# Performance work log

Measured on AMD Instinct MI355X. Metric: run time of the kernel, lower is better.

Reference implementation:

```python
import jax, jax.numpy as jnp
import numpy as np

NUM_HEADS = 16
SIZE_PER_HEAD = 64
NEG_INF = -10000.0

def setup_inputs() -> dict:
    key = jax.random.key(0)
    ks = jax.random.split(key, 4)
    B, S, D = 4, 2048, 1024
    x = jax.random.normal(ks[0], (B, S, D), dtype=jnp.float32)
    mask = jnp.ones((B, S), dtype=jnp.int32)
    std = 0.02
    Wq = jax.random.normal(ks[1], (D, NUM_HEADS * SIZE_PER_HEAD), dtype=jnp.float32) * std
    Wk = jax.random.normal(ks[2], (D, NUM_HEADS * SIZE_PER_HEAD), dtype=jnp.float32) * std
    Wv = jax.random.normal(ks[3], (D, NUM_HEADS * SIZE_PER_HEAD), dtype=jnp.float32) * std
    bq = jnp.zeros((NUM_HEADS * SIZE_PER_HEAD,), dtype=jnp.float32)
    bk = jnp.zeros((NUM_HEADS * SIZE_PER_HEAD,), dtype=jnp.float32)
    bv = jnp.zeros((NUM_HEADS * SIZE_PER_HEAD,), dtype=jnp.float32)
    return {"x": x, "mask": mask, "Wq": Wq, "bq": bq, "Wk": Wk, "bk": bk, "Wv": Wv, "bv": bv}

def reference(x, mask, Wq, bq, Wk, bk, Wv, bv):
    B, S, D = x.shape
    H, Dh = NUM_HEADS, SIZE_PER_HEAD
    # QKV projections (no activations: query/key/value_activation default None)
    q = (x @ Wq + bq).reshape(B, S, H, Dh).transpose(0, 2, 1, 3)  # [B,H,S,Dh]
    k = (x @ Wk + bk).reshape(B, S, H, Dh).transpose(0, 2, 1, 3)
    v = (x @ Wv + bv).reshape(B, S, H, Dh).transpose(0, 2, 1, 3)
    scores = jnp.einsum('bhqd,bhkd->bhqk', q, k) / jnp.sqrt(jnp.float32(Dh))  # [B,H,S,S]
    # additive mask: (1 - mask) * neg_inf, broadcast over heads and query dim
    adder = (1.0 - mask.astype(jnp.float32))[:, None, None, :] * NEG_INF
    probs = jax.nn.softmax(scores + adder, axis=-1)
    # dropout is identity at inference (training=None)
    ctx = jnp.einsum('bhqk,bhkd->bhqd', probs, v)  # [B,H,S,Dh]
    return ctx.transpose(0, 2, 1, 3).reshape(B, S, H * Dh)
```

## Files before the change

kernel.cpp:

```cpp
#include <hip/hip_runtime.h>


typedef __attribute__((ext_vector_type(8))) short bf16x8;
typedef __attribute__((ext_vector_type(4))) float f32x4;
typedef __attribute__((ext_vector_type(16))) float f32x16;

#define LOG2E 1.4426950408889634f

__device__ __forceinline__ ushort f2bf(float f) {
  union { float f; unsigned int u; } x; x.f = f;
  unsigned int r = x.u + 0x7fffu + ((x.u >> 16) & 1u);
  return (ushort)(r >> 16);
}

__device__ __forceinline__ void gload16(const ushort* g, ushort* l) {
  __builtin_amdgcn_global_load_lds(
      (__attribute__((address_space(1))) unsigned int*)(g),
      (__attribute__((address_space(3))) unsigned int*)(l), 16, 0, 0);
}

__global__ __launch_bounds__(256) void prep(
    const float* __restrict__ x, ushort* __restrict__ xb,
    const float* __restrict__ Wq, const float* __restrict__ Wk,
    const float* __restrict__ Wv, ushort* __restrict__ WT,
    const int* __restrict__ mask, int* __restrict__ flagw) {
  __shared__ float tile[32][33];
  __shared__ int accum[64];
  const int blk = blockIdx.x, t = threadIdx.x;
  if (blk < 8192) {
    int i = blk * 256 + t;
    float4 v = ((const float4*)x)[i];
    ushort4 o;
    o.x = f2bf(v.x); o.y = f2bf(v.y); o.z = f2bf(v.z); o.w = f2bf(v.w);
    ((ushort4*)xb)[i] = o;
  } else if (blk < 11264) {
    int bb = blk - 8192;
    int z = bb >> 10, rem = bb & 1023, db = rem >> 5, nb = rem & 31;
    const float* W = (z == 0) ? Wq : ((z == 1) ? Wk : Wv);
    int tx = t & 31, ty = t >> 5;
#pragma unroll
    for (int i = 0; i < 4; i++) {
      int dl = ty + i * 8;
      tile[dl][tx] = W[(size_t)(db * 32 + dl) * 1024 + nb * 32 + tx];
    }
    __syncthreads();
#pragma unroll
    for (int i = 0; i < 4; i++) {
      int nl = ty + i * 8;
      WT[(size_t)(z * 1024 + nb * 32 + nl) * 1024 + db * 32 + tx] = f2bf(tile[tx][nl]);
    }
  } else {
    if (t < 64) accum[t] = 0;
    __syncthreads();
    int p = t >> 2, j = t & 3;
    int base = p * 128 + j * 32;
    int s = 0;
#pragma unroll
    for (int i = 0; i < 8; i++) {
      int4 v = *(const int4*)(mask + base + i * 4);
      s += v.x + v.y + v.z + v.w;
    }
    atomicAdd(&accum[p], s);
    __syncthreads();
    if (t < 4) {
      int w = 0;
#pragma unroll
      for (int kt = 0; kt < 16; kt++)
        if (accum[t * 16 + kt] != 128) w |= (1 << kt);
      flagw[t] = w;
    }
  }
}

__global__ __launch_bounds__(256, 2) void gemm_qkv(
    const ushort* __restrict__ xb, const ushort* __restrict__ WT,
    const float* __restrict__ bq, const float* __restrict__ bk,
    const float* __restrict__ bv, ushort* __restrict__ Qg,
    ushort* __restrict__ Kg, ushort* __restrict__ VTg) {
  __shared__ __align__(16) ushort As[128 * 64];
  __shared__ __align__(16) ushort Bs[128 * 64];
  const int t = threadIdx.x, wid = t >> 6, lane = t & 63;
  const int blk = blockIdx.x;
  int mode, mb, nb;
  const ushort *A, *B;
  if (blk < 1024) {
    mode = 0;
    int lin2 = (blk & 7) * 128 + (blk >> 3);
    nb = lin2 & 15; mb = lin2 >> 4;
    A = xb; B = WT;
  } else {
    mode = 1;
    int l = blk - 1024;
    int lin2 = (l & 7) * 64 + (l >> 3);
    mb = lin2 & 7; nb = lin2 >> 3;
    A = WT + (size_t)2048 * 1024; B = xb;
  }
  const ushort* Ab = A + (size_t)mb * 128 * 1024;
  const ushort* Bb = B + (size_t)nb * 128 * 1024;
  const int wr = wid >> 1, wc = wid & 1;

  f32x4 acc[4][4] = {};

  const int srow = lane >> 3;
  const int schunk = (lane & 7) ^ srow;

#pragma unroll
  for (int i = 0; i < 4; i++) {
    int blki = i * 4 + wid;
    int row = blki * 8 + srow;
    int ldso = __builtin_amdgcn_readfirstlane(blki * 512);
    gload16(Ab + (size_t)row * 1024 + schunk * 8, As + ldso);
    gload16(Bb + (size_t)row * 1024 + schunk * 8, Bs + ldso);
  }

  for (int kt = 0; kt < 16; ++kt) {
    __syncthreads();

    bf16x8 af[2][4], bf[2][4];
#pragma unroll
    for (int ks = 0; ks < 2; ks++) {
#pragma unroll
      for (int m = 0; m < 4; m++) {
        int row = wr * 64 + m * 16 + (lane & 15);
        int slot = (ks * 4 + (lane >> 4)) ^ (row & 7);
        af[ks][m] = *(const bf16x8*)(As + row * 64 + slot * 8);
      }
#pragma unroll
      for (int n = 0; n < 4; n++) {
        int row = wc * 64 + n * 16 + (lane & 15);
        int slot = (ks * 4 + (lane >> 4)) ^ (row & 7);
        bf[ks][n] = *(const bf16x8*)(Bs + row * 64 + slot * 8);
      }
    }
    __syncthreads();

    if (kt < 15) {
      const int kof = (kt + 1) * 64 + schunk * 8;
#pragma unroll
      for (int i = 0; i < 4; i++) {
        int blki = i * 4 + wid;
        int row = blki * 8 + srow;
        int ldso = __builtin_amdgcn_readfirstlane(blki * 512);
        gload16(Ab + (size_t)row * 1024 + kof, As + ldso);
        gload16(Bb + (size_t)row * 1024 + kof, Bs + ldso);
      }
    }

#pragma unroll
    for (int ks = 0; ks < 2; ks++)
#pragma unroll
      for (int m = 0; m < 4; m++)
#pragma unroll
        for (int n = 0; n < 4; n++)
          acc[m][n] = __builtin_amdgcn_mfma_f32_16x16x32_bf16(
              af[ks][m], bf[ks][n], acc[m][n], 0, 0, 0);
  }

#pragma unroll
  for (int m = 0; m < 4; m++) {
#pragma unroll
    for (int n = 0; n < 4; n++) {
      if (mode == 0) {
        int col = nb * 128 + wc * 64 + n * 16 + (lane & 15);
        int wq = col >> 10;
        float bs = wq ? bk[col & 1023] : bq[col & 1023];
        float scale = wq ? 1.0f : (0.125f * LOG2E);
        ushort* dst = wq ? Kg : Qg;
        int h = (col >> 6) & 15, d = col & 63;
#pragma unroll
        for (int r = 0; r < 4; r++) {
          int row = mb * 128 + wr * 64 + m * 16 + (lane >> 4) * 4 + r;
          int b = row >> 11, s = row & 2047;
          float v = (acc[m][n][r] + bs) * scale;
          dst[((size_t)((b << 4) + h) * 2048 + s) * 64 + d] = f2bf(v);
        }
      } else {
        int col = nb * 128 + wc * 64 + n * 16 + (lane & 15);
        int b = col >> 11, s = col & 2047;
#pragma unroll
        for (int r = 0; r < 4; r++) {
          int p = mb * 128 + wr * 64 + m * 16 + (lane >> 4) * 4 + r;
          float v = acc[m][n][r] + bv[p];
          int h = p >> 6, d = p & 63;
          VTg[((size_t)((b << 4) + h) * 64 + d) * 2048 + s] = f2bf(v);
        }
      }
    }
  }
}

__global__ __launch_bounds__(256, 3) void attn_kernel(
    const ushort* __restrict__ Qg, const ushort* __restrict__ Kg,
    const ushort* __restrict__ VTg, const int* __restrict__ mask,
    const int* __restrict__ flagw, float* __restrict__ out) {
  __shared__ __align__(16) ushort Ks[128 * 64];
  __shared__ __align__(16) ushort Vs[64 * 128];
  __shared__ float maddv[128];

  const int t = threadIdx.x, wid = t >> 6, lane = t & 63;
  const int l31 = lane & 31, hi = lane >> 5;
  const int lin = blockIdx.x;
  const int lin2 = (lin & 7) * 128 + (lin >> 3);
  const int qb = lin2 & 15, bh = lin2 >> 4;
  const int b = bh >> 4, h = bh & 15;
  const ushort* Qbh = Qg + ((size_t)bh * 2048 + qb * 128) * 64;
  const ushort* Kbh = Kg + (size_t)bh * 2048 * 64;
  const ushort* Vbh = VTg + (size_t)bh * 64 * 2048;

  const int pr_l = lane >> 4;
  const int s_l = lane & 15;

  const int prq = l31 >> 1;
  const int halfq = l31 & 1;
  const int pr14 = prq & 15;

#pragma unroll
  for (int i = 0; i < 4; i++) {
    int blki = i * 4 + wid;
    int ldso = __builtin_amdgcn_readfirstlane(blki * 512);
    int pr = blki * 4 + pr_l;
    int sp = s_l ^ (pr & 15);
    gload16(Qbh + (size_t)(2 * pr + (sp >> 3)) * 64 + (sp & 7) * 8, Ks + ldso);
  }
  const int fb = flagw[b];
  __syncthreads();
  bf16x8 qf[4];
  {
    const ushort* qbase = Ks + (wid * 16 + prq) * 128;
#pragma unroll
    for (int ds = 0; ds < 4; ds++) {
      int slot = ((ds * 2 + hi) | (halfq << 3)) ^ pr14;
      qf[ds] = *(const bf16x8*)(qbase + slot * 8);
    }
  }
  __syncthreads();

  const f32x16 fzero = {};
  f32x16 cacc[2] = {};
  float l0 = 0.f, l1 = 0.f, l2 = 0.f, l3 = 0.f;

  for (int kt = 0; kt < 16; ++kt) {
    {
#pragma unroll
      for (int i = 0; i < 4; i++) {
        int blki = i * 4 + wid;
        int ldso = __builtin_amdgcn_readfirstlane(blki * 512);
        int pr = blki * 4 + pr_l;
        int sp = s_l ^ (pr & 15);
        gload16(Kbh + (size_t)(kt * 128 + 2 * pr + (sp >> 3)) * 64 + (sp & 7) * 8,
                Ks + ldso);
      }
      int d_l = lane >> 4, c_s = lane & 15;
#pragma unroll
      for (int i = 0; i < 4; i++) {
        int blki = i * 4 + wid;
        int ldso = __builtin_amdgcn_readfirstlane(blki * 512);
        int d = blki * 4 + d_l;
        int cvg = c_s ^ (d & 15);
        gload16(Vbh + (size_t)d * 2048 + kt * 128 + cvg * 8, Vs + ldso);
      }
    }
    const bool msk = ((fb >> kt) & 1) != 0;
    if (msk && t < 128)
      maddv[t] = (1.0f - (float)mask[b * 2048 + kt * 128 + t]) * (-10000.0f * LOG2E);
    __syncthreads();

#pragma unroll
    for (int kb = 0; kb < 4; kb++) {
      const ushort* krow = Ks + (kb * 16 + prq) * 128;
      __builtin_amdgcn_s_setprio(1);
      bf16x8 kf0 = *(const bf16x8*)(krow + (((0 + hi) | (halfq << 3)) ^ pr14) * 8);
      f32x16 a = __builtin_amdgcn_mfma_f32_32x32x16_bf16(kf0, qf[0], fzero, 0, 0, 0);
      bf16x8 kf1 = *(const bf16x8*)(krow + (((2 + hi) | (halfq << 3)) ^ pr14) * 8);
      a = __builtin_amdgcn_mfma_f32_32x32x16_bf16(kf1, qf[1], a, 0, 0, 0);
      bf16x8 kf2 = *(const bf16x8*)(krow + (((4 + hi) | (halfq << 3)) ^ pr14) * 8);
      a = __builtin_amdgcn_mfma_f32_32x32x16_bf16(kf2, qf[2], a, 0, 0, 0);
      bf16x8 kf3 = *(const bf16x8*)(krow + (((6 + hi) | (halfq << 3)) ^ pr14) * 8);
      a = __builtin_amdgcn_mfma_f32_32x32x16_bf16(kf3, qf[3], a, 0, 0, 0);
      __builtin_amdgcn_s_setprio(0);

      if (msk) {
#pragma unroll
        for (int qd = 0; qd < 4; qd++) {
          f32x4 ma = *(const f32x4*)(maddv + kb * 32 + qd * 8 + hi * 4);
#pragma unroll
          for (int rr = 0; rr < 4; rr++) a[qd * 4 + rr] += ma[rr];
        }
      }

#pragma unroll
      for (int w2 = 0; w2 < 2; w2++) {
        const int o = w2 * 8;
        float e0 = __builtin_amdgcn_exp2f(a[o + 0]);
        float e1 = __builtin_amdgcn_exp2f(a[o + 1]);
        float e2 = __builtin_amdgcn_exp2f(a[o + 2]);
        float e3 = __builtin_amdgcn_exp2f(a[o + 3]);
        float e4 = __builtin_amdgcn_exp2f(a[o + 4]);
        float e5 = __builtin_amdgcn_exp2f(a[o + 5]);
        float e6 = __builtin_amdgcn_exp2f(a[o + 6]);
        float e7 = __builtin_amdgcn_exp2f(a[o + 7]);
        l0 += e0; l1 += e1; l2 += e2; l3 += e3;
        l0 += e4; l1 += e5; l2 += e6; l3 += e7;
        unsigned a0, a1, b0, b1;
        asm("v_cvt_pk_bf16_f32 %0, %1, %2" : "=v"(a0) : "v"(e0), "v"(e1));
        asm("v_cvt_pk_bf16_f32 %0, %1, %2" : "=v"(a1) : "v"(e2), "v"(e3));
        asm("v_cvt_pk_bf16_f32 %0, %1, %2" : "=v"(b0) : "v"(e4), "v"(e5));
        asm("v_cvt_pk_bf16_f32 %0, %1, %2" : "=v"(b1) : "v"(e6), "v"(e7));
        asm("v_permlane32_swap_b32 %0, %1" : "+v"(a0), "+v"(b0));
        asm("v_permlane32_swap_b32 %0, %1" : "+v"(a1), "+v"(b1));
        union { unsigned u[4]; bf16x8 v8; } pu;
        pu.u[0] = a0; pu.u[1] = a1; pu.u[2] = b0; pu.u[3] = b1;
        bf16x8 pf = pu.v8;
        int w = kb * 2 + w2;
        __builtin_amdgcn_s_setprio(1);
#pragma unroll
        for (int df = 0; df < 2; df++) {
          int d = df * 32 + l31;
          int c = (w * 2 + hi) ^ (d & 15);
          bf16x8 vf = *(const bf16x8*)(Vs + d * 128 + c * 8);
          cacc[df] = __builtin_amdgcn_mfma_f32_32x32x16_bf16(vf, pf, cacc[df], 0, 0, 0);
        }
        __builtin_amdgcn_s_setprio(0);
      }
    }
    __syncthreads();
  }

  float lrun = (l0 + l1) + (l2 + l3);
  lrun += __shfl_xor(lrun, 32);
  float linv = 1.0f / lrun;
  int qg = qb * 128 + wid * 32 + l31;
  float* op = out + ((size_t)(b * 2048 + qg)) * 1024 + h * 64;
#pragma unroll
  for (int df = 0; df < 2; df++)
#pragma unroll
    for (int qd = 0; qd < 4; qd++) {
      f32x4 v;
      v[0] = cacc[df][qd * 4 + 0] * linv;
      v[1] = cacc[df][qd * 4 + 1] * linv;
      v[2] = cacc[df][qd * 4 + 2] * linv;
      v[3] = cacc[df][qd * 4 + 3] * linv;
      *(f32x4*)(op + df * 32 + qd * 8 + hi * 4) = v;
    }
}

extern "C" void kernel_launch(void* const* d_in, const int* in_sizes, int n_in,
                              void* d_out, int out_size, void* d_ws, size_t ws_size,
                              hipStream_t stream) {
  const float* x  = (const float*)d_in[0];
  const int* mask = (const int*)d_in[1];
  const float* Wq = (const float*)d_in[2];
  const float* bq = (const float*)d_in[3];
  const float* Wk = (const float*)d_in[4];
  const float* bk = (const float*)d_in[5];
  const float* Wv = (const float*)d_in[6];
  const float* bv = (const float*)d_in[7];
  float* out = (float*)d_out;

  char* ws = (char*)d_ws;
  ushort* xb  = (ushort*)(ws);
  ushort* WT  = (ushort*)(ws + (size_t)16777216);
  ushort* Qg  = (ushort*)(ws + (size_t)23068672);
  ushort* Kg  = (ushort*)(ws + (size_t)39845888);
  ushort* VTg = (ushort*)(ws + (size_t)56623104);
  int*    flg = (int*)(ws + (size_t)73400320);

  prep<<<dim3(11265), dim3(256), 0, stream>>>(x, xb, Wq, Wk, Wv, WT, mask, flg);
  gemm_qkv<<<dim3(1536), dim3(256), 0, stream>>>(xb, WT, bq, bk, bv, Qg, Kg, VTg);
  attn_kernel<<<dim3(1024), dim3(256), 0, stream>>>(Qg, Kg, VTg, mask, flg, out);
}
```

Baseline: 155.9 us.

## Prefetch next K/V tile into registers to overlap loads with compute

Replaces the direct global-to-LDS loads of K and V at the start of each tile with register-staged prefetching. The next tile is loaded into registers while the MFMA work on the current tile runs, then written to LDS after a barrier. The aim is to hide global memory latency behind compute. In exchange it costs extra VGPRs for the staging buffers and adds explicit LDS stores, which may reduce occupancy.

```diff
diff --git a/kernel.cpp b/kernel.cpp
--- a/kernel.cpp
+++ b/kernel.cpp
@@ -209,6 +209,10 @@
 
   const int pr_l = lane >> 4;
   const int s_l = lane & 15;
+  const int spk = s_l ^ (4 * wid + pr_l);
+  const int okl = 512 * wid + 128 * pr_l + (spk >> 3) * 64 + (spk & 7) * 8;
+  const int ovl = 8192 * wid + 2048 * pr_l + spk * 8;
+  const int lwr = 512 * wid + lane * 8;
 
   const int prq = l31 >> 1;
   const int halfq = l31 & 1;
@@ -222,6 +226,13 @@
     int sp = s_l ^ (pr & 15);
     gload16(Qbh + (size_t)(2 * pr + (sp >> 3)) * 64 + (sp & 7) * 8, Ks + ldso);
   }
+  bf16x8 kst[4], vst[4];
+#pragma unroll
+  for (int i = 0; i < 4; i++)
+    kst[i] = *(const bf16x8*)(Kbh + 2048 * i + okl);
+#pragma unroll
+  for (int i = 0; i < 4; i++)
+    vst[i] = *(const bf16x8*)(Vbh + 32768 * i + ovl);
   const int fb = flagw[b];
   __syncthreads();
   bf16x8 qf[4];
@@ -234,36 +245,29 @@
     }
   }
   __syncthreads();
+#pragma unroll
+  for (int i = 0; i < 4; i++) *(bf16x8*)(Ks + 2048 * i + lwr) = kst[i];
+#pragma unroll
+  for (int i = 0; i < 4; i++) *(bf16x8*)(Vs + 2048 * i + lwr) = vst[i];
+  if (((fb >> 0) & 1) && t < 128)
+    maddv[t] = (1.0f - (float)mask[b * 2048 + t]) * (-10000.0f * LOG2E);
 
   const f32x16 fzero = {};
   f32x16 cacc[2] = {};
   float l0 = 0.f, l1 = 0.f, l2 = 0.f, l3 = 0.f;
 
   for (int kt = 0; kt < 16; ++kt) {
-    {
-#pragma unroll
-      for (int i = 0; i < 4; i++) {
-        int blki = i * 4 + wid;
-        int ldso = __builtin_amdgcn_readfirstlane(blki * 512);
-        int pr = blki * 4 + pr_l;
-        int sp = s_l ^ (pr & 15);
-        gload16(Kbh + (size_t)(kt * 128 + 2 * pr + (sp >> 3)) * 64 + (sp & 7) * 8,
-                Ks + ldso);
-      }
-      int d_l = lane >> 4, c_s = lane & 15;
-#pragma unroll
-      for (int i = 0; i < 4; i++) {
-        int blki = i * 4 + wid;
-        int ldso = __builtin_amdgcn_readfirstlane(blki * 512);
-        int d = blki * 4 + d_l;
-        int cvg = c_s ^ (d & 15);
-        gload16(Vbh + (size_t)d * 2048 + kt * 128 + cvg * 8, Vs + ldso);
-      }
+    __syncthreads();
+
+    if (kt < 15) {
+#pragma unroll
+      for (int i = 0; i < 4; i++)
+        kst[i] = *(const bf16x8*)(Kbh + (size_t)(kt + 1) * 8192 + 2048 * i + okl);
+#pragma unroll
+      for (int i = 0; i < 4; i++)
+        vst[i] = *(const bf16x8*)(Vbh + 32768 * i + (kt + 1) * 128 + ovl);
     }
     const bool msk = ((fb >> kt) & 1) != 0;
-    if (msk && t < 128)
-      maddv[t] = (1.0f - (float)mask[b * 2048 + kt * 128 + t]) * (-10000.0f * LOG2E);
-    __syncthreads();
 
 #pragma unroll
     for (int kb = 0; kb < 4; kb++) {
@@ -323,7 +327,16 @@
         __builtin_amdgcn_s_setprio(0);
       }
     }
-    __syncthreads();
+
+    if (kt < 15) {
+      __syncthreads();
+#pragma unroll
+      for (int i = 0; i < 4; i++) *(bf16x8*)(Ks + 2048 * i + lwr) = kst[i];
+#pragma unroll
+      for (int i = 0; i < 4; i++) *(bf16x8*)(Vs + 2048 * i + lwr) = vst[i];
+      if (((fb >> (kt + 1)) & 1) && t < 128)
+        maddv[t] = (1.0f - (float)mask[b * 2048 + (kt + 1) * 128 + t]) * (-10000.0f * LOG2E);
+    }
   }
 
   float lrun = (l0 + l1) + (l2 + l3);
```

Measured after the change: 220.0 us. 41.1% more time.

## Double-buffer K/V tiles in attention kernel to overlap loads with compute

Applied to the files above, without the earlier changes.

Adds a second LDS buffer for the K, V and mask-adder tiles. The next tile's global-to-LDS loads are issued before computing on the current one, and the per-iteration pre-compute barrier is removed. This should hide global load latency behind the MFMA and exp work. LDS use doubles, so the occupancy hint drops from 3 to 2 blocks per CU.

```diff
diff --git a/kernel.cpp b/kernel.cpp
--- a/kernel.cpp
+++ b/kernel.cpp
@@ -189,13 +189,13 @@
   }
 }
 
-__global__ __launch_bounds__(256, 3) void attn_kernel(
+__global__ __launch_bounds__(256, 2) void attn_kernel(
     const ushort* __restrict__ Qg, const ushort* __restrict__ Kg,
     const ushort* __restrict__ VTg, const int* __restrict__ mask,
     const int* __restrict__ flagw, float* __restrict__ out) {
-  __shared__ __align__(16) ushort Ks[128 * 64];
-  __shared__ __align__(16) ushort Vs[64 * 128];
-  __shared__ float maddv[128];
+  __shared__ __align__(16) ushort Ks[2][128 * 64];
+  __shared__ __align__(16) ushort Vs[2][64 * 128];
+  __shared__ float maddv[2][128];
 
   const int t = threadIdx.x, wid = t >> 6, lane = t & 63;
   const int l31 = lane & 31, hi = lane >> 5;
@@ -220,13 +220,21 @@
     int ldso = __builtin_amdgcn_readfirstlane(blki * 512);
     int pr = blki * 4 + pr_l;
     int sp = s_l ^ (pr & 15);
-    gload16(Qbh + (size_t)(2 * pr + (sp >> 3)) * 64 + (sp & 7) * 8, Ks + ldso);
+    gload16(Qbh + (size_t)(2 * pr + (sp >> 3)) * 64 + (sp & 7) * 8,
+            &Ks[0][0] + ldso);
+    gload16(Kbh + (size_t)(2 * pr + (sp >> 3)) * 64 + (sp & 7) * 8,
+            &Ks[1][0] + ldso);
+    int d = blki * 4 + pr_l;
+    int cvg = s_l ^ (d & 15);
+    gload16(Vbh + (size_t)d * 2048 + cvg * 8, &Vs[1][0] + ldso);
   }
   const int fb = flagw[b];
+  if (((fb >> 0) & 1) && t < 128)
+    maddv[1][t] = (1.0f - (float)mask[b * 2048 + t]) * (-10000.0f * LOG2E);
   __syncthreads();
   bf16x8 qf[4];
   {
-    const ushort* qbase = Ks + (wid * 16 + prq) * 128;
+    const ushort* qbase = &Ks[0][0] + (wid * 16 + prq) * 128;
 #pragma unroll
     for (int ds = 0; ds < 4; ds++) {
       int slot = ((ds * 2 + hi) | (halfq << 3)) ^ pr14;
@@ -240,34 +248,34 @@
   float l0 = 0.f, l1 = 0.f, l2 = 0.f, l3 = 0.f;
 
   for (int kt = 0; kt < 16; ++kt) {
-    {
+    const int bufc = (kt + 1) & 1;
+    const int bufn = bufc ^ 1;
+
+    if (kt < 15) {
 #pragma unroll
       for (int i = 0; i < 4; i++) {
         int blki = i * 4 + wid;
         int ldso = __builtin_amdgcn_readfirstlane(blki * 512);
         int pr = blki * 4 + pr_l;
         int sp = s_l ^ (pr & 15);
-        gload16(Kbh + (size_t)(kt * 128 + 2 * pr + (sp >> 3)) * 64 + (sp & 7) * 8,
-                Ks + ldso);
-      }
-      int d_l = lane >> 4, c_s = lane & 15;
-#pragma unroll
-      for (int i = 0; i < 4; i++) {
-        int blki = i * 4 + wid;
-        int ldso = __builtin_amdgcn_readfirstlane(blki * 512);
-        int d = blki * 4 + d_l;
-        int cvg = c_s ^ (d & 15);
-        gload16(Vbh + (size_t)d * 2048 + kt * 128 + cvg * 8, Vs + ldso);
-      }
+        gload16(Kbh + (size_t)((kt + 1) * 128 + 2 * pr + (sp >> 3)) * 64 + (sp & 7) * 8,
+                &Ks[bufn][0] + ldso);
+        int d = blki * 4 + pr_l;
+        int cvg = s_l ^ (d & 15);
+        gload16(Vbh + (size_t)d * 2048 + (kt + 1) * 128 + cvg * 8,
+                &Vs[bufn][0] + ldso);
+      }
+      if (((fb >> (kt + 1)) & 1) && t < 128)
+        maddv[bufn][t] =
+            (1.0f - (float)mask[b * 2048 + (kt + 1) * 128 + t]) * (-10000.0f * LOG2E);
     }
     const bool msk = ((fb >> kt) & 1) != 0;
-    if (msk && t < 128)
-      maddv[t] = (1.0f - (float)mask[b * 2048 + kt * 128 + t]) * (-10000.0f * LOG2E);
-    __syncthreads();
+    const ushort* Ksb = &Ks[bufc][0];
+    const ushort* Vsb = &Vs[bufc][0];
 
 #pragma unroll
     for (int kb = 0; kb < 4; kb++) {
-      const ushort* krow = Ks + (kb * 16 + prq) * 128;
+      const ushort* krow = Ksb + (kb * 16 + prq) * 128;
       __builtin_amdgcn_s_setprio(1);
       bf16x8 kf0 = *(const bf16x8*)(krow + (((0 + hi) | (halfq << 3)) ^ pr14) * 8);
       f32x16 a = __builtin_amdgcn_mfma_f32_32x32x16_bf16(kf0, qf[0], fzero, 0, 0, 0);
@@ -282,7 +290,7 @@
       if (msk) {
 #pragma unroll
         for (int qd = 0; qd < 4; qd++) {
-          f32x4 ma = *(const f32x4*)(maddv + kb * 32 + qd * 8 + hi * 4);
+          f32x4 ma = *(const f32x4*)(&maddv[bufc][0] + kb * 32 + qd * 8 + hi * 4);
 #pragma unroll
           for (int rr = 0; rr < 4; rr++) a[qd * 4 + rr] += ma[rr];
         }
@@ -317,13 +325,14 @@
         for (int df = 0; df < 2; df++) {
           int d = df * 32 + l31;
           int c = (w * 2 + hi) ^ (d & 15);
-          bf16x8 vf = *(const bf16x8*)(Vs + d * 128 + c * 8);
+          bf16x8 vf = *(const bf16x8*)(Vsb + d * 128 + c * 8);
           cacc[df] = __builtin_amdgcn_mfma_f32_32x32x16_bf16(vf, pf, cacc[df], 0, 0, 0);
         }
         __builtin_amdgcn_s_setprio(0);
       }
     }
-    __syncthreads();
+
+    if (kt < 15) __syncthreads();
   }
 
   float lrun = (l0 + l1) + (l2 + l3);
```

Result: no change. 157.8 us (+1.2%).

## Software-pipeline QK and softmax-PV blocks with double score accumulators

Applied to the files above, without the earlier changes.

Inside each key tile, the QK MFMA for the next 32-key block is now issued before the exp/PV work of the previous block, using two score accumulators so matrix and vector work can overlap. Q fragments are loaded straight from global memory into registers instead of being staged through shared memory, which removes two barriers. The K and V global-to-LDS loads are merged into one loop, and the trailing barrier is skipped on the last tile. Launch bounds drop from 3 to 2 waves-per-SIMD minimum to make room for the extra accumulator registers, which can lower occupancy.

```diff
diff --git a/kernel.cpp b/kernel.cpp
--- a/kernel.cpp
+++ b/kernel.cpp
@@ -189,7 +189,69 @@
   }
 }
 
-__global__ __launch_bounds__(256, 3) void attn_kernel(
+
+#define QK_BLOCK(AOUT, KB)                                                     \
+  {                                                                            \
+    const ushort* krow = Ks + ((KB) * 16 + prq) * 128;                         \
+    __builtin_amdgcn_s_setprio(1);                                             \
+    bf16x8 kf0 = *(const bf16x8*)(krow + (((0 + hi) | (halfq << 3)) ^ pr14) * 8); \
+    AOUT = __builtin_amdgcn_mfma_f32_32x32x16_bf16(kf0, qf[0], fzero, 0, 0, 0);\
+    bf16x8 kf1 = *(const bf16x8*)(krow + (((2 + hi) | (halfq << 3)) ^ pr14) * 8); \
+    AOUT = __builtin_amdgcn_mfma_f32_32x32x16_bf16(kf1, qf[1], AOUT, 0, 0, 0); \
+    bf16x8 kf2 = *(const bf16x8*)(krow + (((4 + hi) | (halfq << 3)) ^ pr14) * 8); \
+    AOUT = __builtin_amdgcn_mfma_f32_32x32x16_bf16(kf2, qf[2], AOUT, 0, 0, 0); \
+    bf16x8 kf3 = *(const bf16x8*)(krow + (((6 + hi) | (halfq << 3)) ^ pr14) * 8); \
+    AOUT = __builtin_amdgcn_mfma_f32_32x32x16_bf16(kf3, qf[3], AOUT, 0, 0, 0); \
+    __builtin_amdgcn_s_setprio(0);                                             \
+  }
+
+#define FIN_BLOCK(AIN, KB)                                                     \
+  {                                                                            \
+    if (msk) {                                                                 \
+      _Pragma("unroll")                                                        \
+      for (int qd = 0; qd < 4; qd++) {                                         \
+        f32x4 ma = *(const f32x4*)(maddv + (KB) * 32 + qd * 8 + hi * 4);       \
+        _Pragma("unroll")                                                      \
+        for (int rr = 0; rr < 4; rr++) AIN[qd * 4 + rr] += ma[rr];             \
+      }                                                                        \
+    }                                                                          \
+    _Pragma("unroll")                                                          \
+    for (int w2 = 0; w2 < 2; w2++) {                                           \
+      const int o = w2 * 8;                                                    \
+      float e0 = __builtin_amdgcn_exp2f(AIN[o + 0]);                           \
+      float e1 = __builtin_amdgcn_exp2f(AIN[o + 1]);                           \
+      float e2 = __builtin_amdgcn_exp2f(AIN[o + 2]);                           \
+      float e3 = __builtin_amdgcn_exp2f(AIN[o + 3]);                           \
+      float e4 = __builtin_amdgcn_exp2f(AIN[o + 4]);                           \
+      float e5 = __builtin_amdgcn_exp2f(AIN[o + 5]);                           \
+      float e6 = __builtin_amdgcn_exp2f(AIN[o + 6]);                           \
+      float e7 = __builtin_amdgcn_exp2f(AIN[o + 7]);                           \
+      l0 += e0; l1 += e1; l2 += e2; l3 += e3;                                  \
+      l0 += e4; l1 += e5; l2 += e6; l3 += e7;                                  \
+      unsigned a0, a1, b0, b1;                                                 \
+      asm("v_cvt_pk_bf16_f32 %0, %1, %2" : "=v"(a0) : "v"(e0), "v"(e1));       \
+      asm("v_cvt_pk_bf16_f32 %0, %1, %2" : "=v"(a1) : "v"(e2), "v"(e3));       \
+      asm("v_cvt_pk_bf16_f32 %0, %1, %2" : "=v"(b0) : "v"(e4), "v"(e5));       \
+      asm("v_cvt_pk_bf16_f32 %0, %1, %2" : "=v"(b1) : "v"(e6), "v"(e7));       \
+      asm("v_permlane32_swap_b32 %0, %1" : "+v"(a0), "+v"(b0));                \
+      asm("v_permlane32_swap_b32 %0, %1" : "+v"(a1), "+v"(b1));                \
+      union { unsigned u[4]; bf16x8 v8; } pu;                                  \
+      pu.u[0] = a0; pu.u[1] = a1; pu.u[2] = b0; pu.u[3] = b1;                  \
+      bf16x8 pf = pu.v8;                                                       \
+      const int w = (KB) * 2 + w2;                                             \
+      __builtin_amdgcn_s_setprio(1);                                           \
+      _Pragma("unroll")                                                        \
+      for (int df = 0; df < 2; df++) {                                         \
+        int d = df * 32 + l31;                                                 \
+        int c = (w * 2 + hi) ^ (d & 15);                                       \
+        bf16x8 vf = *(const bf16x8*)(Vs + d * 128 + c * 8);                    \
+        cacc[df] = __builtin_amdgcn_mfma_f32_32x32x16_bf16(vf, pf, cacc[df], 0, 0, 0); \
+      }                                                                        \
+      __builtin_amdgcn_s_setprio(0);                                           \
+    }                                                                          \
+  }
+
+__global__ __launch_bounds__(256, 2) void attn_kernel(
     const ushort* __restrict__ Qg, const ushort* __restrict__ Kg,
     const ushort* __restrict__ VTg, const int* __restrict__ mask,
     const int* __restrict__ flagw, float* __restrict__ out) {
@@ -214,116 +276,48 @@
   const int halfq = l31 & 1;
   const int pr14 = prq & 15;
 
-#pragma unroll
-  for (int i = 0; i < 4; i++) {
-    int blki = i * 4 + wid;
-    int ldso = __builtin_amdgcn_readfirstlane(blki * 512);
-    int pr = blki * 4 + pr_l;
-    int sp = s_l ^ (pr & 15);
-    gload16(Qbh + (size_t)(2 * pr + (sp >> 3)) * 64 + (sp & 7) * 8, Ks + ldso);
-  }
-  const int fb = flagw[b];
-  __syncthreads();
   bf16x8 qf[4];
   {
-    const ushort* qbase = Ks + (wid * 16 + prq) * 128;
-#pragma unroll
-    for (int ds = 0; ds < 4; ds++) {
-      int slot = ((ds * 2 + hi) | (halfq << 3)) ^ pr14;
-      qf[ds] = *(const bf16x8*)(qbase + slot * 8);
-    }
-  }
-  __syncthreads();
+    const ushort* qrow = Qbh + (size_t)(wid * 32 + l31) * 64 + hi * 8;
+#pragma unroll
+    for (int ds = 0; ds < 4; ds++)
+      qf[ds] = *(const bf16x8*)(qrow + ds * 16);
+  }
+  const int fb = flagw[b];
 
   const f32x16 fzero = {};
   f32x16 cacc[2] = {};
   float l0 = 0.f, l1 = 0.f, l2 = 0.f, l3 = 0.f;
 
   for (int kt = 0; kt < 16; ++kt) {
-    {
-#pragma unroll
-      for (int i = 0; i < 4; i++) {
-        int blki = i * 4 + wid;
-        int ldso = __builtin_amdgcn_readfirstlane(blki * 512);
-        int pr = blki * 4 + pr_l;
-        int sp = s_l ^ (pr & 15);
-        gload16(Kbh + (size_t)(kt * 128 + 2 * pr + (sp >> 3)) * 64 + (sp & 7) * 8,
-                Ks + ldso);
-      }
-      int d_l = lane >> 4, c_s = lane & 15;
-#pragma unroll
-      for (int i = 0; i < 4; i++) {
-        int blki = i * 4 + wid;
-        int ldso = __builtin_amdgcn_readfirstlane(blki * 512);
-        int d = blki * 4 + d_l;
-        int cvg = c_s ^ (d & 15);
-        gload16(Vbh + (size_t)d * 2048 + kt * 128 + cvg * 8, Vs + ldso);
-      }
+#pragma unroll
+    for (int i = 0; i < 4; i++) {
+      int blki = i * 4 + wid;
+      int ldso = __builtin_amdgcn_readfirstlane(blki * 512);
+      int pr = blki * 4 + pr_l;
+      int sp = s_l ^ (pr & 15);
+      gload16(Kbh + (size_t)(kt * 128 + 2 * pr + (sp >> 3)) * 64 + (sp & 7) * 8,
+              Ks + ldso);
+      int d = blki * 4 + pr_l;
+      int cvg = s_l ^ (d & 15);
+      gload16(Vbh + (size_t)d * 2048 + kt * 128 + cvg * 8, Vs + ldso);
     }
     const bool msk = ((fb >> kt) & 1) != 0;
     if (msk && t < 128)
       maddv[t] = (1.0f - (float)mask[b * 2048 + kt * 128 + t]) * (-10000.0f * LOG2E);
     __syncthreads();
 
-#pragma unroll
-    for (int kb = 0; kb < 4; kb++) {
-      const ushort* krow = Ks + (kb * 16 + prq) * 128;
-      __builtin_amdgcn_s_setprio(1);
-      bf16x8 kf0 = *(const bf16x8*)(krow + (((0 + hi) | (halfq << 3)) ^ pr14) * 8);
-      f32x16 a = __builtin_amdgcn_mfma_f32_32x32x16_bf16(kf0, qf[0], fzero, 0, 0, 0);
-      bf16x8 kf1 = *(const bf16x8*)(krow + (((2 + hi) | (halfq << 3)) ^ pr14) * 8);
-      a = __builtin_amdgcn_mfma_f32_32x32x16_bf16(kf1, qf[1], a, 0, 0, 0);
-      bf16x8 kf2 = *(const bf16x8*)(krow + (((4 + hi) | (halfq << 3)) ^ pr14) * 8);
-      a = __builtin_amdgcn_mfma_f32_32x32x16_bf16(kf2, qf[2], a, 0, 0, 0);
-      bf16x8 kf3 = *(const bf16x8*)(krow + (((6 + hi) | (halfq << 3)) ^ pr14) * 8);
-      a = __builtin_amdgcn_mfma_f32_32x32x16_bf16(kf3, qf[3], a, 0, 0, 0);
-      __builtin_amdgcn_s_setprio(0);
-
-      if (msk) {
-#pragma unroll
-        for (int qd = 0; qd < 4; qd++) {
-          f32x4 ma = *(const f32x4*)(maddv + kb * 32 + qd * 8 + hi * 4);
-#pragma unroll
-          for (int rr = 0; rr < 4; rr++) a[qd * 4 + rr] += ma[rr];
-        }
-      }
-
-#pragma unroll
-      for (int w2 = 0; w2 < 2; w2++) {
-        const int o = w2 * 8;
-        float e0 = __builtin_amdgcn_exp2f(a[o + 0]);
-        float e1 = __builtin_amdgcn_exp2f(a[o + 1]);
-        float e2 = __builtin_amdgcn_exp2f(a[o + 2]);
-        float e3 = __builtin_amdgcn_exp2f(a[o + 3]);
-        float e4 = __builtin_amdgcn_exp2f(a[o + 4]);
-        float e5 = __builtin_amdgcn_exp2f(a[o + 5]);
-        float e6 = __builtin_amdgcn_exp2f(a[o + 6]);
-        float e7 = __builtin_amdgcn_exp2f(a[o + 7]);
-        l0 += e0; l1 += e1; l2 += e2; l3 += e3;
-        l0 += e4; l1 += e5; l2 += e6; l3 += e7;
-        unsigned a0, a1, b0, b1;
-        asm("v_cvt_pk_bf16_f32 %0, %1, %2" : "=v"(a0) : "v"(e0), "v"(e1));
-        asm("v_cvt_pk_bf16_f32 %0, %1, %2" : "=v"(a1) : "v"(e2), "v"(e3));
-        asm("v_cvt_pk_bf16_f32 %0, %1, %2" : "=v"(b0) : "v"(e4), "v"(e5));
-        asm("v_cvt_pk_bf16_f32 %0, %1, %2" : "=v"(b1) : "v"(e6), "v"(e7));
-        asm("v_permlane32_swap_b32 %0, %1" : "+v"(a0), "+v"(b0));
-        asm("v_permlane32_swap_b32 %0, %1" : "+v"(a1), "+v"(b1));
-        union { unsigned u[4]; bf16x8 v8; } pu;
-        pu.u[0] = a0; pu.u[1] = a1; pu.u[2] = b0; pu.u[3] = b1;
-        bf16x8 pf = pu.v8;
-        int w = kb * 2 + w2;
-        __builtin_amdgcn_s_setprio(1);
-#pragma unroll
-        for (int df = 0; df < 2; df++) {
-          int d = df * 32 + l31;
-          int c = (w * 2 + hi) ^ (d & 15);
-          bf16x8 vf = *(const bf16x8*)(Vs + d * 128 + c * 8);
-          cacc[df] = __builtin_amdgcn_mfma_f32_32x32x16_bf16(vf, pf, cacc[df], 0, 0, 0);
-        }
-        __builtin_amdgcn_s_setprio(0);
-      }
-    }
-    __syncthreads();
+    f32x16 aA, aB;
+    QK_BLOCK(aA, 0)
+    QK_BLOCK(aB, 1)
+    FIN_BLOCK(aA, 0)
+    QK_BLOCK(aA, 2)
+    FIN_BLOCK(aB, 1)
+    QK_BLOCK(aB, 3)
+    FIN_BLOCK(aA, 2)
+    FIN_BLOCK(aB, 3)
+
+    if (kt < 15) __syncthreads();
   }
 
   float lrun = (l0 + l1) + (l2 + l3);
```

After: 155.0 us. About the same (-0.6%).
